# Performance work log

Hardware: AMD Instinct MI355X
Metric: run time of the kernel (lower is better)

Reference implementation:

```python
import jax, jax.numpy as jnp
import numpy as np

FS = 2          # filter_size (kernel == stride, non-overlapping)
NL = 10         # num_layers
C_IN = 3        # input_channels
H = 256         # hidden width
OUT = 10        # out_dim
B = 128         # batch
D = FS ** NL    # input spatial length = 1024


def setup_inputs() -> dict:
    key = jax.random.key(0)
    ks = jax.random.split(key, NL + 2)
    inp = {"x": jax.random.normal(ks[0], (B, C_IN, D), dtype=jnp.float32)}
    cin = C_IN
    for l in range(NL):
        dl = D // FS ** (l + 1)  # out positions at layer l
        inp[f"w{l}"] = jax.random.normal(ks[l + 1], (H, cin, dl, FS), dtype=jnp.float32)
        cin = H
    inp["beta"] = jax.random.normal(ks[-1], (H, OUT), dtype=jnp.float32)
    return inp


def _lc(x, w):
    # Locally-connected 1d, stride == kernel: unfold is a pure reshape.
    # x: (B, C, Dd*k), w: (O, C, Dd, k) -> out: (B, O, Dd)
    O, C, Dd, k = w.shape
    xu = x.reshape(x.shape[0], C, Dd, k)
    # per-position contraction over (C, k); avoids the (B,O,C,Dd,k) intermediate
    return jnp.einsum('bcdk,ocdk->bod', xu, w) / (C ** 0.5)


def reference(x, w0, w1, w2, w3, w4, w5, w6, w7, w8, w9, beta):
    ws = [w0, w1, w2, w3, w4, w5, w6, w7, w8, w9]
    y = x
    for w in ws:  # fixed small layer loop
        y = jax.nn.relu(_lc(y, w))
    y = y.mean(axis=-1)            # (B, H) — last spatial dim is size 1
    return y @ beta / beta.shape[0]  # (B, OUT)
```

## Files before the change

### kernel.cpp

```cpp
#include <hip/hip_runtime.h>
#include <hip/hip_bf16.h>
#include <stdint.h>


typedef __attribute__((ext_vector_type(4))) float floatx4;
typedef __attribute__((ext_vector_type(8))) short shortx8;

__device__ __forceinline__ float bf2f(unsigned short u){
    union { unsigned int u; float f; } c; c.u = ((unsigned int)u) << 16; return c.f;
}
__device__ __forceinline__ unsigned short f2bf(float f){
    union { float f; unsigned int u; } c; c.f = f;
    unsigned int x = c.u;
    x += 0x7FFFu + ((x >> 16) & 1u);
    return (unsigned short)(x >> 16);
}

__global__ void probe_kernel(const unsigned int* __restrict__ x, int* __restrict__ flag){
    __shared__ int cnt[256];
    int tid = threadIdx.x;
    unsigned short lo = (unsigned short)(x[tid] & 0xFFFFu);
    int e = (lo >> 7) & 0xFF;
    cnt[tid] = (e >= 90 && e <= 143) ? 1 : 0;
    __syncthreads();
    for (int s = 128; s > 0; s >>= 1){
        if (tid < s) cnt[tid] += cnt[tid + s];
        __syncthreads();
    }
    if (tid == 0) *flag = (cnt[0] > 160) ? 1 : 0;
}

__global__ __launch_bounds__(256) void l0_kernel(const int* __restrict__ flag,
        const void* __restrict__ xv, const void* __restrict__ wv,
        unsigned short* __restrict__ A1){
    __shared__ float Xs[128*6];
    const int d = blockIdx.x;
    const int tid = threadIdx.x;
    const bool BF = (*flag != 0);
    for (int i = tid; i < 384; i += 256){
        int b = i / 3, c = i - b*3;
        if (BF){
            unsigned int u = *(const unsigned int*)((const unsigned short*)xv + (b*3+c)*1024 + 2*d);
            Xs[b*6 + c*2]     = bf2f((unsigned short)(u & 0xFFFFu));
            Xs[b*6 + c*2 + 1] = bf2f((unsigned short)(u >> 16));
        } else {
            const float* xf = (const float*)xv + (b*3+c)*1024 + 2*d;
            Xs[b*6 + c*2] = xf[0]; Xs[b*6 + c*2 + 1] = xf[1];
        }
    }
    __syncthreads();
    const int o = tid;
    float wr[6];
    #pragma unroll
    for (int c = 0; c < 3; ++c){
        if (BF){
            unsigned int u = *(const unsigned int*)((const unsigned short*)wv + ((o*3+c)*512 + d)*2);
            wr[c*2]   = bf2f((unsigned short)(u & 0xFFFFu));
            wr[c*2+1] = bf2f((unsigned short)(u >> 16));
        } else {
            const float* wf = (const float*)wv + ((o*3+c)*512 + d)*2;
            wr[c*2] = wf[0]; wr[c*2+1] = wf[1];
        }
    }
    const float s3 = 0.57735026918962576f;
    for (int b = 0; b < 128; ++b){
        float s = 0.f;
        #pragma unroll
        for (int j = 0; j < 6; ++j) s += Xs[b*6 + j] * wr[j];
        A1[d*32768 + b*256 + o] = f2bf(fmaxf(s, 0.f) * s3);
    }
}

template<bool WBF, bool ATOMIC>
__device__ __forceinline__ void layer_main_impl(const unsigned short* __restrict__ Ain,
        const void* __restrict__ wv, void* __restrict__ out, int dl, int ks,
        unsigned short* __restrict__ Wt0, unsigned short* __restrict__ Wt1){
    const int tid  = threadIdx.x;
    const int lane = tid & 63, wv_ = tid >> 6;
    const int g = lane >> 4, mr = lane & 15;
    const int nd = dl >> 2;

    int dg, ng, mh, ksid;
    {
        const int bi = blockIdx.x;
        const int G  = gridDim.x;
        if (nd >= 2 && (G & 127) == 0){
            const int x = bi & 7, j = (bi >> 3) & 15, gg = bi >> 7;
            const int pid = gg*8 + x;
            const int nd2 = nd >> 1;
            dg   = (pid % nd2)*2 + (j & 1);
            ng   = (j >> 1) & 3;
            mh   = j >> 3;
            ksid = pid / nd2;
        } else {
            dg = bi % nd; const int r = bi / nd;
            ng = r & 3; mh = (r >> 2) & 1; ksid = r >> 3;
        }
    }
    const int TS = 16 / ks;
    const int d0 = dg << 2;
    const int o0 = ng << 6;
    const int b0 = mh << 6;
    const int dme = d0 + wv_;
    const float* wF = (const float*)wv;
    const unsigned short* wB = (const unsigned short*)wv;

    const int cl  = tid & 15;
    const int ooB = tid >> 4;
    const int ws0 = (((o0 + ooB      )*256 + cl)*dl + d0)*2;
    const int ws1 = (((o0 + ooB + 16 )*256 + cl)*dl + d0)*2;
    const int ws2 = (((o0 + ooB + 32 )*256 + cl)*dl + d0)*2;
    const int ws3 = (((o0 + ooB + 48 )*256 + cl)*dl + d0)*2;
    const int wcstep = 32*dl;

    const unsigned short* Ab = Ain + (2*dme + (g>>1))*32768 + (b0 + mr)*256 + (g&1)*8;
    const int c_base = ksid*TS;

    floatx4 acc[4][4];
    #pragma unroll
    for (int m = 0; m < 4; ++m)
        #pragma unroll
        for (int nb = 0; nb < 4; ++nb)
            acc[m][nb] = (floatx4){0.f,0.f,0.f,0.f};

    shortx8 a0, a1, a2, a3;
    shortx8 n0, n1, n2, n3;
    uint4  u0, u1, u2, u3;
    float4 wa0, wa1, wa2, wa3;
    float4 wb0, wb1, wb2, wb3;

#define LOADA4(d0_,d1_,d2_,d3_,s_) do { \
    const unsigned short* _p = Ab + ((c_base + (s_)) << 4); \
    d0_ = *(const shortx8*)(_p);          \
    d1_ = *(const shortx8*)(_p + 4096);   \
    d2_ = *(const shortx8*)(_p + 8192);   \
    d3_ = *(const shortx8*)(_p + 12288);  \
} while(0)

#define LOADW(s_) do { \
    const int _c = (c_base + (s_)) * wcstep; \
    if (WBF){ \
        u0 = *(const uint4*)(wB + ws0 + _c); \
        u1 = *(const uint4*)(wB + ws1 + _c); \
        u2 = *(const uint4*)(wB + ws2 + _c); \
        u3 = *(const uint4*)(wB + ws3 + _c); \
    } else { \
        wa0 = *(const float4*)(wF + ws0 + _c); wb0 = *(const float4*)(wF + ws0 + _c + 4); \
        wa1 = *(const float4*)(wF + ws1 + _c); wb1 = *(const float4*)(wF + ws1 + _c + 4); \
        wa2 = *(const float4*)(wF + ws2 + _c); wb2 = *(const float4*)(wF + ws2 + _c + 4); \
        wa3 = *(const float4*)(wF + ws3 + _c); wb3 = *(const float4*)(wF + ws3 + _c + 4); \
    } \
} while(0)

#define STW_RR(Wt_, uu_, fa_, fb_, oo_) do { \
    unsigned short w0_,w1_,w2_,w3_,w4_,w5_,w6_,w7_; \
    if (WBF){ const unsigned short* _pu = (const unsigned short*)&(uu_); \
        w0_=_pu[0]; w1_=_pu[1]; w2_=_pu[2]; w3_=_pu[3]; w4_=_pu[4]; w5_=_pu[5]; w6_=_pu[6]; w7_=_pu[7]; \
    } else { \
        w0_=f2bf((fa_).x); w1_=f2bf((fa_).y); w2_=f2bf((fa_).z); w3_=f2bf((fa_).w); \
        w4_=f2bf((fb_).x); w5_=f2bf((fb_).y); w6_=f2bf((fb_).z); w7_=f2bf((fb_).w); \
    } \
    (Wt_)[((0*64) + (oo_))*40 +  0 + cl] = w0_;   \
    (Wt_)[((0*64) + (oo_))*40 + 16 + cl] = w1_;   \
    (Wt_)[((1*64) + (oo_))*40 +  0 + cl] = w2_; \
    (Wt_)[((1*64) + (oo_))*40 + 16 + cl] = w3_; \
    (Wt_)[((2*64) + (oo_))*40 +  0 + cl] = w4_; \
    (Wt_)[((2*64) + (oo_))*40 + 16 + cl] = w5_; \
    (Wt_)[((3*64) + (oo_))*40 +  0 + cl] = w6_; \
    (Wt_)[((3*64) + (oo_))*40 + 16 + cl] = w7_; \
} while(0)

#define STOREW(Wt_) do { \
    STW_RR(Wt_, u0, wa0, wb0, ooB      ); \
    STW_RR(Wt_, u1, wa1, wb1, ooB + 16 ); \
    STW_RR(Wt_, u2, wa2, wb2, ooB + 32 ); \
    STW_RR(Wt_, u3, wa3, wb3, ooB + 48 ); \
} while(0)

    LOADW(0);
    LOADA4(a0, a1, a2, a3, 0);
    STOREW(Wt0);

    for (int s = 0; s < TS; ++s){
        __syncthreads();
        if (s + 1 < TS){
            LOADA4(n0, n1, n2, n3, s + 1);
            LOADW(s + 1);
        }
        const unsigned short* Wr = (s & 1) ? Wt1 : Wt0;
        shortx8 br0 = *(const shortx8*)(Wr + (wv_*64 +  0 + mr)*40 + g*8);
        shortx8 br1 = *(const shortx8*)(Wr + (wv_*64 + 16 + mr)*40 + g*8);
        shortx8 br2 = *(const shortx8*)(Wr + (wv_*64 + 32 + mr)*40 + g*8);
        shortx8 br3 = *(const shortx8*)(Wr + (wv_*64 + 48 + mr)*40 + g*8);
#define MFMA_ROW(m_, ar_) \
        acc[m_][0] = __builtin_amdgcn_mfma_f32_16x16x32_bf16(ar_, br0, acc[m_][0], 0,0,0); \
        acc[m_][1] = __builtin_amdgcn_mfma_f32_16x16x32_bf16(ar_, br1, acc[m_][1], 0,0,0); \
        acc[m_][2] = __builtin_amdgcn_mfma_f32_16x16x32_bf16(ar_, br2, acc[m_][2], 0,0,0); \
        acc[m_][3] = __builtin_amdgcn_mfma_f32_16x16x32_bf16(ar_, br3, acc[m_][3], 0,0,0);
        MFMA_ROW(0, a0)
        MFMA_ROW(1, a1)
        MFMA_ROW(2, a2)
        MFMA_ROW(3, a3)
#undef MFMA_ROW
        if (s + 1 < TS){
            STOREW((s & 1) ? Wt0 : Wt1);
            a0 = n0; a1 = n1; a2 = n2; a3 = n3;
        }
    }
#undef LOADA4
#undef LOADW
#undef STW_RR
#undef STOREW

    #pragma unroll
    for (int m = 0; m < 4; ++m)
        #pragma unroll
        for (int nb = 0; nb < 4; ++nb)
            #pragma unroll
            for (int r = 0; r < 4; ++r){
                const int bb = b0 + m*16 + g*4 + r;
                const int oc = o0 + nb*16 + mr;
                if (ATOMIC)
                    unsafeAtomicAdd((float*)out + (dme*128 + bb)*256 + oc, acc[m][nb][r]);
                else
                    ((unsigned short*)out)[dme*32768 + bb*256 + oc] =
                        f2bf(fmaxf(acc[m][nb][r], 0.f) * 0.0625f);
            }
}

template<bool ATOMIC>
__global__ __launch_bounds__(256,2) void layer_main_k(const int* __restrict__ flag,
        const unsigned short* __restrict__ Ain, const void* __restrict__ wv,
        void* __restrict__ out, int dl, int ks){
    __shared__ unsigned short Wt[2][4*64*40];
    if (*flag) layer_main_impl<true,  ATOMIC>(Ain, wv, out, dl, ks, Wt[0], Wt[1]);
    else       layer_main_impl<false, ATOMIC>(Ain, wv, out, dl, ks, Wt[0], Wt[1]);
}

template<bool WBF>
__device__ __forceinline__ void tail_impl(const unsigned short* __restrict__ Ain,
        const void* __restrict__ wv, float* __restrict__ outS, int dl, int ksplit){
    int id = blockIdx.x;
    int d = id % dl; int t2 = id / dl;
    int ob = t2 & 3; int ksid = t2 >> 2;
    const int KSEG = 512 / ksplit;
    const int k0s = ksid * KSEG;
    const int lane = threadIdx.x & 63, wv2 = threadIdx.x >> 6;
    const int mr = lane & 15, kg = lane >> 4;
    const float* wF = (const float*)wv;
    const unsigned short* wB = (const unsigned short*)wv;
    floatx4 acc[2][4];
    #pragma unroll
    for (int mi = 0; mi < 2; ++mi)
        #pragma unroll
        for (int ni = 0; ni < 4; ++ni) acc[mi][ni] = (floatx4){0.f,0.f,0.f,0.f};
    for (int k0 = k0s; k0 < k0s + KSEG; k0 += 32){
        int c0 = (k0 >> 1) + kg*4;
        shortx8 af[2];
        #pragma unroll
        for (int mi = 0; mi < 2; ++mi){
            int b = wv2*32 + mi*16 + mr;
            #pragma unroll
            for (int cc = 0; cc < 4; ++cc){
                af[mi][2*cc]   = (short)Ain[(2*d)*32768   + b*256 + c0 + cc];
                af[mi][2*cc+1] = (short)Ain[(2*d+1)*32768 + b*256 + c0 + cc];
            }
        }
        shortx8 bf_[4];
        #pragma unroll
        for (int ni = 0; ni < 4; ++ni){
            int o = ob*64 + ni*16 + mr;
            int base = ((o*256 + c0)*dl + d)*2;
            #pragma unroll
            for (int cc = 0; cc < 4; ++cc){
                if (WBF){
                    unsigned int u = *(const unsigned int*)(wB + base);
                    bf_[ni][2*cc]   = (short)(u & 0xFFFFu);
                    bf_[ni][2*cc+1] = (short)(u >> 16);
                } else {
                    bf_[ni][2*cc]   = (short)f2bf(wF[base]);
                    bf_[ni][2*cc+1] = (short)f2bf(wF[base+1]);
                }
                base += 2*dl;
            }
        }
        #pragma unroll
        for (int mi = 0; mi < 2; ++mi)
            #pragma unroll
            for (int ni = 0; ni < 4; ++ni)
                acc[mi][ni] = __builtin_amdgcn_mfma_f32_16x16x32_bf16(af[mi], bf_[ni], acc[mi][ni], 0,0,0);
    }
    #pragma unroll
    for (int mi = 0; mi < 2; ++mi)
        #pragma unroll
        for (int ni = 0; ni < 4; ++ni)
            #pragma unroll
            for (int r = 0; r < 4; ++r){
                int b = wv2*32 + mi*16 + kg*4 + r;
                int o = ob*64 + ni*16 + mr;
                unsafeAtomicAdd(outS + (d*128 + b)*256 + o, acc[mi][ni][r]);
            }
}
__global__ __launch_bounds__(256) void tail_k(const int* __restrict__ flag,
        const unsigned short* __restrict__ Ain, const void* __restrict__ wv,
        float* __restrict__ outS, int dl, int ksplit){
    if (*flag) tail_impl<true >(Ain, wv, outS, dl, ksplit);
    else       tail_impl<false>(Ain, wv, outS, dl, ksplit);
}

__global__ __launch_bounds__(256) void fin_kernel(const float* __restrict__ S,
        unsigned short* __restrict__ A, int n){
    int i = (blockIdx.x*256 + threadIdx.x)*4;
    if (i + 3 < n){
        float4 v = *(const float4*)(S + i);
        unsigned short r0 = f2bf(fmaxf(v.x,0.f)*0.0625f);
        unsigned short r1 = f2bf(fmaxf(v.y,0.f)*0.0625f);
        unsigned short r2 = f2bf(fmaxf(v.z,0.f)*0.0625f);
        unsigned short r3 = f2bf(fmaxf(v.w,0.f)*0.0625f);
        unsigned int lo = (unsigned int)r0 | ((unsigned int)r1 << 16);
        unsigned int hi = (unsigned int)r2 | ((unsigned int)r3 << 16);
        uint2 u; u.x = lo; u.y = hi;
        *(uint2*)(A + i) = u;
    }
}

template<bool BF>
__device__ __forceinline__ void epi_impl(const float* __restrict__ S9, const void* __restrict__ beta,
                                         void* __restrict__ out){
    int b = blockIdx.x;
    int lane = threadIdx.x;
    float accv[10];
    #pragma unroll
    for (int o = 0; o < 10; ++o) accv[o] = 0.f;
    for (int h = lane; h < 256; h += 64){
        float y = fmaxf(S9[b*256 + h], 0.f) * 0.0625f;
        #pragma unroll
        for (int o = 0; o < 10; ++o){
            float be = BF ? bf2f(((const unsigned short*)beta)[h*10 + o])
                          : ((const float*)beta)[h*10 + o];
            accv[o] += y * be;
        }
    }
    #pragma unroll
    for (int off = 32; off > 0; off >>= 1){
        #pragma unroll
        for (int o = 0; o < 10; ++o)
            accv[o] += __shfl_down(accv[o], off, 64);
    }
    if (lane == 0){
        #pragma unroll
        for (int o = 0; o < 10; ++o){
            float v = accv[o] * (1.f/256.f);
            if (BF) ((unsigned short*)out)[b*10 + o] = f2bf(v);
            else    ((float*)out)[b*10 + o] = v;
        }
    }
}
__global__ void epi_kernel(const int* __restrict__ flag, const float* __restrict__ S9,
                           const void* __restrict__ beta, void* __restrict__ out){
    if (*flag) epi_impl<true>(S9, beta, out);
    else       epi_impl<false>(S9, beta, out);
}

extern "C" void kernel_launch(void* const* d_in, const int* in_sizes, int n_in,
                              void* d_out, int out_size, void* d_ws, size_t ws_size,
                              hipStream_t stream) {
    (void)in_sizes; (void)n_in; (void)out_size; (void)ws_size;
    char* wsb = (char*)d_ws;
    int* flag = (int*)wsb;
    unsigned short* A1 = (unsigned short*)(wsb + 512);
    float* S2 = (float*)(wsb + 512);
    float* S3 = S2 + 4194304;
    float* S4 = S3 + 2097152;
    float* S5 = S4 + 1048576;
    float* S6 = S5 + 524288;
    float* S7 = S6 + 262144;
    float* S8 = S7 + 131072;
    float* S9 = S8 + 65536;
    unsigned short* A2 = (unsigned short*)(wsb + 512 + 33554432);
    unsigned short* A3 = A2;
    unsigned short* A4 = A3 + 4194304;
    unsigned short* A5 = A4 + 2097152;
    unsigned short* A6 = A5 + 1048576;
    unsigned short* A7 = A6 + 524288;
    unsigned short* A8 = A7 + 262144;
    unsigned short* A9 = A8 + 131072;

    probe_kernel<<<1, 256, 0, stream>>>((const unsigned int*)d_in[0], flag);
    l0_kernel<<<512, 256, 0, stream>>>(flag, d_in[0], d_in[1], A1);
    layer_main_k<false><<<512, 256, 0, stream>>>(flag, A1, d_in[2], A2, 256, 1);
    hipMemsetAsync(S2, 0, 33423360, stream);
    layer_main_k<true ><<<512, 256, 0, stream>>>(flag, A2, d_in[3], S2, 128, 2);
    fin_kernel<<<4096, 256, 0, stream>>>(S2, A3, 4194304);
    layer_main_k<true ><<<512, 256, 0, stream>>>(flag, A3, d_in[4], S3, 64, 4);
    fin_kernel<<<2048, 256, 0, stream>>>(S3, A4, 2097152);
    layer_main_k<true ><<<512, 256, 0, stream>>>(flag, A4, d_in[5], S4, 32, 8);
    fin_kernel<<<1024, 256, 0, stream>>>(S4, A5, 1048576);
    layer_main_k<true ><<<512, 256, 0, stream>>>(flag, A5, d_in[6], S5, 16, 16);
    fin_kernel<<<512, 256, 0, stream>>>(S5, A6, 524288);
    layer_main_k<true ><<<256, 256, 0, stream>>>(flag, A6, d_in[7], S6, 8, 16);
    fin_kernel<<<256, 256, 0, stream>>>(S6, A7, 262144);
    layer_main_k<true ><<<128, 256, 0, stream>>>(flag, A7, d_in[8], S7, 4, 16);
    fin_kernel<<<128, 256, 0, stream>>>(S7, A8, 131072);
    tail_k<<<128, 256, 0, stream>>>(flag, A8, d_in[9], S8, 2, 16);
    fin_kernel<<<64, 256, 0, stream>>>(S8, A9, 65536);
    tail_k<<<64, 256, 0, stream>>>(flag, A9, d_in[10], S9, 1, 16);
    epi_kernel<<<128, 64, 0, stream>>>(flag, S9, d_in[11], d_out);
}
```

Measured before the change: 635.3 us.

## Replace split-K atomic accumulation with per-split partial buffers reduced in finalize

Split-K layers now write their fp32 partial sums with plain stores into separate per-split slices of one reused workspace buffer, instead of atomically adding into zeroed accumulators. The finalize kernels and the epilogue sum the ks partial slices before applying ReLU and scaling. This removes the large memset and the atomic traffic. In exchange, the finalize step reads ks times more data, and the workspace slices must fit in the reused region.

```diff
diff --git a/kernel.cpp b/kernel.cpp
--- a/kernel.cpp
+++ b/kernel.cpp
@@ -71,7 +71,7 @@
     }
 }
 
-template<bool WBF, bool ATOMIC>
+template<bool WBF, bool PARTIAL>
 __device__ __forceinline__ void layer_main_impl(const unsigned short* __restrict__ Ain,
         const void* __restrict__ wv, void* __restrict__ out, int dl, int ks,
         unsigned short* __restrict__ Wt0, unsigned short* __restrict__ Wt1){
@@ -212,6 +212,7 @@
 #undef STW_RR
 #undef STOREW
 
+    const size_t pofs = PARTIAL ? ((size_t)ksid * ((size_t)dl << 15)) : 0;
     #pragma unroll
     for (int m = 0; m < 4; ++m)
         #pragma unroll
@@ -220,26 +221,26 @@
             for (int r = 0; r < 4; ++r){
                 const int bb = b0 + m*16 + g*4 + r;
                 const int oc = o0 + nb*16 + mr;
-                if (ATOMIC)
-                    unsafeAtomicAdd((float*)out + (dme*128 + bb)*256 + oc, acc[m][nb][r]);
+                if (PARTIAL)
+                    ((float*)out)[pofs + (size_t)(dme*128 + bb)*256 + oc] = acc[m][nb][r];
                 else
                     ((unsigned short*)out)[dme*32768 + bb*256 + oc] =
                         f2bf(fmaxf(acc[m][nb][r], 0.f) * 0.0625f);
             }
 }
 
-template<bool ATOMIC>
+template<bool PARTIAL>
 __global__ __launch_bounds__(256,2) void layer_main_k(const int* __restrict__ flag,
         const unsigned short* __restrict__ Ain, const void* __restrict__ wv,
         void* __restrict__ out, int dl, int ks){
     __shared__ unsigned short Wt[2][4*64*40];
-    if (*flag) layer_main_impl<true,  ATOMIC>(Ain, wv, out, dl, ks, Wt[0], Wt[1]);
-    else       layer_main_impl<false, ATOMIC>(Ain, wv, out, dl, ks, Wt[0], Wt[1]);
+    if (*flag) layer_main_impl<true,  PARTIAL>(Ain, wv, out, dl, ks, Wt[0], Wt[1]);
+    else       layer_main_impl<false, PARTIAL>(Ain, wv, out, dl, ks, Wt[0], Wt[1]);
 }
 
 template<bool WBF>
 __device__ __forceinline__ void tail_impl(const unsigned short* __restrict__ Ain,
-        const void* __restrict__ wv, float* __restrict__ outS, int dl, int ksplit){
+        const void* __restrict__ wv, float* __restrict__ outP, int dl, int ksplit){
     int id = blockIdx.x;
     int d = id % dl; int t2 = id / dl;
     int ob = t2 & 3; int ksid = t2 >> 2;
@@ -290,6 +291,7 @@
             for (int ni = 0; ni < 4; ++ni)
                 acc[mi][ni] = __builtin_amdgcn_mfma_f32_16x16x32_bf16(af[mi], bf_[ni], acc[mi][ni], 0,0,0);
     }
+    const size_t pofs = (size_t)ksid * ((size_t)dl << 15);
     #pragma unroll
     for (int mi = 0; mi < 2; ++mi)
         #pragma unroll
@@ -298,21 +300,25 @@
             for (int r = 0; r < 4; ++r){
                 int b = wv2*32 + mi*16 + kg*4 + r;
                 int o = ob*64 + ni*16 + mr;
-                unsafeAtomicAdd(outS + (d*128 + b)*256 + o, acc[mi][ni][r]);
+                outP[pofs + (size_t)(d*128 + b)*256 + o] = acc[mi][ni][r];
             }
 }
 __global__ __launch_bounds__(256) void tail_k(const int* __restrict__ flag,
         const unsigned short* __restrict__ Ain, const void* __restrict__ wv,
-        float* __restrict__ outS, int dl, int ksplit){
-    if (*flag) tail_impl<true >(Ain, wv, outS, dl, ksplit);
-    else       tail_impl<false>(Ain, wv, outS, dl, ksplit);
-}
-
-__global__ __launch_bounds__(256) void fin_kernel(const float* __restrict__ S,
-        unsigned short* __restrict__ A, int n){
+        float* __restrict__ outP, int dl, int ksplit){
+    if (*flag) tail_impl<true >(Ain, wv, outP, dl, ksplit);
+    else       tail_impl<false>(Ain, wv, outP, dl, ksplit);
+}
+
+__global__ __launch_bounds__(256) void fin_kernel(const float* __restrict__ P,
+        unsigned short* __restrict__ A, int n, int ks){
     int i = (blockIdx.x*256 + threadIdx.x)*4;
     if (i + 3 < n){
-        float4 v = *(const float4*)(S + i);
+        float4 v = *(const float4*)(P + i);
+        for (int k = 1; k < ks; ++k){
+            float4 w = *(const float4*)(P + (size_t)k*n + i);
+            v.x += w.x; v.y += w.y; v.z += w.z; v.w += w.w;
+        }
         unsigned short r0 = f2bf(fmaxf(v.x,0.f)*0.0625f);
         unsigned short r1 = f2bf(fmaxf(v.y,0.f)*0.0625f);
         unsigned short r2 = f2bf(fmaxf(v.z,0.f)*0.0625f);
@@ -325,7 +331,7 @@
 }
 
 template<bool BF>
-__device__ __forceinline__ void epi_impl(const float* __restrict__ S9, const void* __restrict__ beta,
+__device__ __forceinline__ void epi_impl(const float* __restrict__ P9, const void* __restrict__ beta,
                                          void* __restrict__ out){
     int b = blockIdx.x;
     int lane = threadIdx.x;
@@ -333,7 +339,11 @@
     #pragma unroll
     for (int o = 0; o < 10; ++o) accv[o] = 0.f;
     for (int h = lane; h < 256; h += 64){
-        float y = fmaxf(S9[b*256 + h], 0.f) * 0.0625f;
+        float s = 0.f;
+        #pragma unroll
+        for (int k = 0; k < 16; ++k)
+            s += P9[(size_t)k*32768 + b*256 + h];
+        float y = fmaxf(s, 0.f) * 0.0625f;
         #pragma unroll
         for (int o = 0; o < 10; ++o){
             float be = BF ? bf2f(((const unsigned short*)beta)[h*10 + o])
@@ -356,10 +366,10 @@
         }
     }
 }
-__global__ void epi_kernel(const int* __restrict__ flag, const float* __restrict__ S9,
+__global__ void epi_kernel(const int* __restrict__ flag, const float* __restrict__ P9,
                            const void* __restrict__ beta, void* __restrict__ out){
-    if (*flag) epi_impl<true>(S9, beta, out);
-    else       epi_impl<false>(S9, beta, out);
+    if (*flag) epi_impl<true>(P9, beta, out);
+    else       epi_impl<false>(P9, beta, out);
 }
 
 extern "C" void kernel_launch(void* const* d_in, const int* in_sizes, int n_in,
@@ -369,14 +379,7 @@
     char* wsb = (char*)d_ws;
     int* flag = (int*)wsb;
     unsigned short* A1 = (unsigned short*)(wsb + 512);
-    float* S2 = (float*)(wsb + 512);
-    float* S3 = S2 + 4194304;
-    float* S4 = S3 + 2097152;
-    float* S5 = S4 + 1048576;
-    float* S6 = S5 + 524288;
-    float* S7 = S6 + 262144;
-    float* S8 = S7 + 131072;
-    float* S9 = S8 + 65536;
+    float* P = (float*)(wsb + 512);
     unsigned short* A2 = (unsigned short*)(wsb + 512 + 33554432);
     unsigned short* A3 = A2;
     unsigned short* A4 = A3 + 4194304;
@@ -389,21 +392,20 @@
     probe_kernel<<<1, 256, 0, stream>>>((const unsigned int*)d_in[0], flag);
     l0_kernel<<<512, 256, 0, stream>>>(flag, d_in[0], d_in[1], A1);
     layer_main_k<false><<<512, 256, 0, stream>>>(flag, A1, d_in[2], A2, 256, 1);
-    hipMemsetAsync(S2, 0, 33423360, stream);
-    layer_main_k<true ><<<512, 256, 0, stream>>>(flag, A2, d_in[3], S2, 128, 2);
-    fin_kernel<<<4096, 256, 0, stream>>>(S2, A3, 4194304);
-    layer_main_k<true ><<<512, 256, 0, stream>>>(flag, A3, d_in[4], S3, 64, 4);
-    fin_kernel<<<2048, 256, 0, stream>>>(S3, A4, 2097152);
-    layer_main_k<true ><<<512, 256, 0, stream>>>(flag, A4, d_in[5], S4, 32, 8);
-    fin_kernel<<<1024, 256, 0, stream>>>(S4, A5, 1048576);
-    layer_main_k<true ><<<512, 256, 0, stream>>>(flag, A5, d_in[6], S5, 16, 16);
-    fin_kernel<<<512, 256, 0, stream>>>(S5, A6, 524288);
-    layer_main_k<true ><<<256, 256, 0, stream>>>(flag, A6, d_in[7], S6, 8, 16);
-    fin_kernel<<<256, 256, 0, stream>>>(S6, A7, 262144);
-    layer_main_k<true ><<<128, 256, 0, stream>>>(flag, A7, d_in[8], S7, 4, 16);
-    fin_kernel<<<128, 256, 0, stream>>>(S7, A8, 131072);
-    tail_k<<<128, 256, 0, stream>>>(flag, A8, d_in[9], S8, 2, 16);
-    fin_kernel<<<64, 256, 0, stream>>>(S8, A9, 65536);
-    tail_k<<<64, 256, 0, stream>>>(flag, A9, d_in[10], S9, 1, 16);
-    epi_kernel<<<128, 64, 0, stream>>>(flag, S9, d_in[11], d_out);
-}
+    layer_main_k<true ><<<512, 256, 0, stream>>>(flag, A2, d_in[3], P, 128, 2);
+    fin_kernel<<<4096, 256, 0, stream>>>(P, A3, 4194304, 2);
+    layer_main_k<true ><<<512, 256, 0, stream>>>(flag, A3, d_in[4], P, 64, 4);
+    fin_kernel<<<2048, 256, 0, stream>>>(P, A4, 2097152, 4);
+    layer_main_k<true ><<<512, 256, 0, stream>>>(flag, A4, d_in[5], P, 32, 8);
+    fin_kernel<<<1024, 256, 0, stream>>>(P, A5, 1048576, 8);
+    layer_main_k<true ><<<512, 256, 0, stream>>>(flag, A5, d_in[6], P, 16, 16);
+    fin_kernel<<<512, 256, 0, stream>>>(P, A6, 524288, 16);
+    layer_main_k<true ><<<256, 256, 0, stream>>>(flag, A6, d_in[7], P, 8, 16);
+    fin_kernel<<<256, 256, 0, stream>>>(P, A7, 262144, 16);
+    layer_main_k<true ><<<128, 256, 0, stream>>>(flag, A7, d_in[8], P, 4, 16);
+    fin_kernel<<<128, 256, 0, stream>>>(P, A8, 131072, 16);
+    tail_k<<<128, 256, 0, stream>>>(flag, A8, d_in[9], P, 2, 16);
+    fin_kernel<<<64, 256, 0, stream>>>(P, A9, 65536, 16);
+    tail_k<<<64, 256, 0, stream>>>(flag, A9, d_in[10], P, 1, 16);
+    epi_kernel<<<128, 64, 0, stream>>>(flag, P, d_in[11], d_out);
+}
```

New measurement: 586.8 us. -7.6%, faster.
